# Kernel optimization log

Hardware: AMD Instinct MI355X
Metric: run time of the kernel (lower is better)

Reference implementation:

```python
import jax, jax.numpy as jnp
import numpy as np

M1 = 32
M2 = 32
S1 = 64
S2 = 64
TWO_PI = jnp.float32(2.0 * np.pi)


def setup_inputs() -> dict:
    key = jax.random.key(0)
    k1, k2, k3, k4, k5 = jax.random.split(key, 5)
    B, C, N = 8, 64, 16384
    x = jax.random.normal(k1, (B, C, N), dtype=jnp.float32)
    x_in = jax.random.uniform(k2, (B, N, 2), dtype=jnp.float32)
    x_out = jax.random.uniform(k3, (B, N, 2), dtype=jnp.float32)
    # xavier_normal for fan_in=64, fan_out=64 over [i,o,m,2]
    std = jnp.float32(np.sqrt(2.0 / (64 + 64)))
    w1 = std * jax.random.normal(k4, (64, 64, M2, 2), dtype=jnp.float32)
    w2 = std * jax.random.normal(k5, (64, 64, M1, 2), dtype=jnp.float32)
    return {"x": x, "x_in": x_in, "x_out": x_out, "w1": w1, "w2": w2}


def reference(x, x_in, x_out, w1, w2):
    # iphi = identity: mapped coords are the mesh coords themselves.
    # Original code repeats the 1-D NUFFT bases along the grid dims (s1/s2)
    # before the einsums; since the repeated axis is constant, the final
    # contraction over it is exactly a factor s1 (resp. s2). We compute the
    # mathematically identical form without materializing [B,N,m,s] tensors.
    Wy = w1[..., 0] + 1j * w1[..., 1]  # [i, o, m2] complex
    Wx = w2[..., 0] + 1j * w2[..., 1]  # [i, o, m1] complex
    ky = jnp.arange(M2, dtype=jnp.float32)
    kx = jnp.arange(M1, dtype=jnp.float32)

    # forward NUFFT bases from x_in  (exp(-i 2 pi k . p))
    bfy = jnp.exp(-1j * TWO_PI * x_in[..., 0:1] * ky)   # [B, N, m2]
    bfx = jnp.exp(-1j * TWO_PI * x_in[..., 1:2] * kx)   # [B, N, m1]
    # inverse NUFFT bases from x_out (exp(+i 2 pi k . p))
    ibfy = jnp.exp(1j * TWO_PI * x_out[..., 0:1] * ky)  # [B, N, m2]
    ibfx = jnp.exp(1j * TWO_PI * x_out[..., 1:2] * kx)  # [B, N, m1]

    xc = x.astype(jnp.complex64)

    # y-direction branch (fourier_weight[0])
    fty = jnp.einsum('bcn,bny->bcy', xc, bfy)           # [B, in, m2]
    my = jnp.einsum('biy,ioy->boy', fty, Wy)            # [B, out, m2]
    xy = S1 * jnp.einsum('boy,bny->bon', my, ibfy).real  # [B, out, N]

    # x-direction branch (fourier_weight[1])
    ftx = jnp.einsum('bcn,bnx->bcx', xc, bfx)           # [B, in, m1]
    mx = jnp.einsum('bix,iox->box', ftx, Wx)            # [B, out, m1]
    xx = S2 * jnp.einsum('box,bnx->bon', mx, ibfx).real  # [B, out, N]

    return xx + xy
```

## Files before the change

kernel.cpp:

```cpp
#include <hip/hip_runtime.h>

#define BB 8
#define CC 64
#define OO 64
#define NN 16384
#define MMODE 32
#define JJ 128
#define SFAC 64.0f

typedef __attribute__((ext_vector_type(8))) short short8;
typedef __attribute__((ext_vector_type(4))) float f32x4;

static __device__ __forceinline__ unsigned short f2bf(float f) {
  unsigned u = __float_as_uint(f);
  u += 0x7FFF + ((u >> 16) & 1);
  return (unsigned short)(u >> 16);
}
static __device__ __forceinline__ unsigned pack2(float a, float b) {
  return (unsigned)f2bf(a) | ((unsigned)f2bf(b) << 16);
}
static __device__ __forceinline__ float sin2pi(float x) { return __builtin_amdgcn_sinf(x); }
static __device__ __forceinline__ float cos2pi(float x) { return __builtin_amdgcn_cosf(x); }


__global__ __launch_bounds__(256) void fwd_kernel(
    const float* __restrict__ x, const float* __restrict__ x_in,
    float* __restrict__ part) {
  __shared__ __attribute__((aligned(16))) short bas[JJ * 72];
  __shared__ __attribute__((aligned(16))) short xs[32 * 72];
  __shared__ __attribute__((aligned(16))) float ps[1024];
  const int t = threadIdx.x;
  const int b = blockIdx.z, chalf = blockIdx.y, sl = blockIdx.x;
  const int n0 = sl * 512;

  {
    const float4 v = *(const float4*)&x_in[((size_t)b * NN + n0) * 2 + t * 4];
    *(float4*)&ps[t * 4] = v;
  }
  const int xc = t >> 3, xng = t & 7;
  const float* xbase = x + ((size_t)(b * CC + chalf * 32 + xc)) * NN + n0 + xng * 4;
  float4 ra = *(const float4*)(xbase);
  float4 rb = *(const float4*)(xbase + 32);

  const int w = t >> 6, L = t & 63;
  const int q4 = L >> 4, l15 = L & 15;
  f32x4 acc[4];
#pragma unroll
  for (int i = 0; i < 4; ++i) acc[i] = (f32x4){0.f, 0.f, 0.f, 0.f};

  __syncthreads();

  for (int s = 0; s < 8; ++s) {
    *(uint2*)&xs[xc * 72 + xng * 4]      = make_uint2(pack2(ra.x, ra.y), pack2(ra.z, ra.w));
    *(uint2*)&xs[xc * 72 + xng * 4 + 32] = make_uint2(pack2(rb.x, rb.y), pack2(rb.z, rb.w));
    if (s < 7) {
      ra = *(const float4*)(xbase + (s + 1) * 64);
      rb = *(const float4*)(xbase + (s + 1) * 64 + 32);
    }
#pragma unroll
    for (int ti = 0; ti < 2; ++ti) {
      const int tau = t + ti * 256;
      const int ng = tau & 7, mm = tau >> 3;
      const int br = mm >> 5, m = mm & 31;
      const float fm = (float)m;
      union { unsigned short u[8]; uint4 v; } R, I;
#pragma unroll
      for (int k = 0; k < 8; ++k) {
        const float p = ps[(s * 64 + ng * 8 + k) * 2 + br];
        float rev = fm * p;
        rev -= floorf(rev);
        R.u[k] = f2bf(cos2pi(rev));
        I.u[k] = f2bf(-sin2pi(rev));
      }
      const int row = br * 64 + 2 * m;
      *(uint4*)&bas[row * 72 + ng * 8]       = R.v;
      *(uint4*)&bas[(row + 1) * 72 + ng * 8] = I.v;
    }
    __syncthreads();
#pragma unroll
    for (int ks = 0; ks < 2; ++ks) {
      const int ko = ks * 32 + q4 * 8;
      const short8 a0 = *(const short8*)&bas[(w * 32 + l15) * 72 + ko];
      const short8 a1 = *(const short8*)&bas[(w * 32 + 16 + l15) * 72 + ko];
      const short8 b0 = *(const short8*)&xs[l15 * 72 + ko];
      const short8 b1 = *(const short8*)&xs[(16 + l15) * 72 + ko];
      acc[0] = __builtin_amdgcn_mfma_f32_16x16x32_bf16(a0, b0, acc[0], 0, 0, 0);
      acc[1] = __builtin_amdgcn_mfma_f32_16x16x32_bf16(a0, b1, acc[1], 0, 0, 0);
      acc[2] = __builtin_amdgcn_mfma_f32_16x16x32_bf16(a1, b0, acc[2], 0, 0, 0);
      acc[3] = __builtin_amdgcn_mfma_f32_16x16x32_bf16(a1, b1, acc[3], 0, 0, 0);
    }
    __syncthreads();
  }
  float* pp = part + (size_t)(b * 32 + sl) * JJ * CC;
  const int jb0 = w * 32 + q4 * 4;
  const int cb = chalf * 32 + l15;
#pragma unroll
  for (int ji = 0; ji < 2; ++ji)
#pragma unroll
    for (int ci = 0; ci < 2; ++ci) {
      const f32x4 v = acc[ji * 2 + ci];
#pragma unroll
      for (int r = 0; r < 4; ++r)
        pp[(jb0 + ji * 16 + r) * CC + cb + ci * 16] = v[r];
    }
}

__global__ __launch_bounds__(256) void mix_kernel(
    const float* __restrict__ part, const float* __restrict__ w1,
    const float* __restrict__ w2, float* __restrict__ A) {
  __shared__ float red[8][64];
  __shared__ float fre[64], fim[64];
  const int m = blockIdx.x, branch = blockIdx.y, b = blockIdx.z;
  const int t = threadIdx.x;
  const int c = t & 63, g = t >> 6;
  const int jb = branch * 64 + 2 * m;
  float pre = 0.f, pim = 0.f;
#pragma unroll
  for (int k = 0; k < 8; ++k) {
    const int sl = g + 4 * k;
    const float* pp = part + (size_t)(b * 32 + sl) * JJ * CC;
    pre += pp[jb * CC + c];
    pim += pp[(jb + 1) * CC + c];
  }
  red[g * 2][c] = pre;
  red[g * 2 + 1][c] = pim;
  __syncthreads();
  if (t < 64) {
    fre[t] = red[0][t] + red[2][t] + red[4][t] + red[6][t];
    fim[t] = red[1][t] + red[3][t] + red[5][t] + red[7][t];
  }
  __syncthreads();
  const float* w = branch ? w2 : w1;
  const int o = c;
  float ar = 0.f, ai = 0.f;
#pragma unroll 4
  for (int ii = 0; ii < 16; ++ii) {
    const int i = g * 16 + ii;
    const float2 wv = *(const float2*)&w[(((size_t)i * 64 + o) * MMODE + m) * 2];
    ar += fre[i] * wv.x - fim[i] * wv.y;
    ai += fre[i] * wv.y + fim[i] * wv.x;
  }
  red[g * 2][o] = ar;
  red[g * 2 + 1][o] = ai;
  __syncthreads();
  if (t < 64) {
    const float sr = red[0][t] + red[2][t] + red[4][t] + red[6][t];
    const float si = red[1][t] + red[3][t] + red[5][t] + red[7][t];
    *(float2*)&A[((size_t)b * OO + t) * JJ + jb] = make_float2(SFAC * sr, -SFAC * si);
  }
}

__global__ __launch_bounds__(256) void inv_kernel(
    const float* __restrict__ x_out, const float* __restrict__ A,
    float* __restrict__ out) {
  __shared__ __attribute__((aligned(16))) short As_s[OO * 136];
  __shared__ __attribute__((aligned(16))) short basn[64 * 136];
  __shared__ __attribute__((aligned(16))) float psI[512];
  const int t = threadIdx.x;
  const int b = blockIdx.y;
  const int n0 = blockIdx.x * 256;

  if (t < 128) {
    const float4 v = *(const float4*)&x_out[((size_t)b * NN + n0) * 2 + t * 4];
    *(float4*)&psI[t * 4] = v;
  }
#pragma unroll
  for (int idx = t; idx < 2048; idx += 256) {
    const int o = idx >> 5, j4 = idx & 31;
    const float4 v = *(const float4*)&A[((size_t)b * OO + o) * JJ + j4 * 4];
    *(uint2*)&As_s[o * 136 + j4 * 4] = make_uint2(pack2(v.x, v.y), pack2(v.z, v.w));
  }
  const int w = t >> 6, L = t & 63;
  const int q4 = L >> 4, l15 = L & 15;
  const int nl = t & 63, q = t >> 6, br = q >> 1, half = q & 1;
  const int ot0 = (w & 1) * 32;
  const int nt0 = (w >> 1) * 32;
  __syncthreads();

  for (int s = 0; s < 4; ++s) {
    {
      const float p = psI[(s * 64 + nl) * 2 + br];
      const float fr = p - floorf(p);
      const float s1 = sin2pi(fr), c1 = cos2pi(fr);
      float brr = 1.f, bii = 0.f;
      if (half) {
        float r = c1, qq = s1;
#pragma unroll
        for (int k = 0; k < 4; ++k) { const float nr = r*r - qq*qq, ni = 2.f*r*qq; r = nr; qq = ni; }
        brr = r; bii = qq;
      }
      short* bp = &basn[nl * 136 + br * 64 + half * 32];
#pragma unroll
      for (int g = 0; g < 4; ++g) {
        union { unsigned short u[8]; uint4 v; } P;
#pragma unroll
        for (int mi = 0; mi < 4; ++mi) {
          P.u[2 * mi]     = f2bf(brr);
          P.u[2 * mi + 1] = f2bf(bii);
          const float nr = brr * c1 - bii * s1, ni = brr * s1 + bii * c1;
          brr = nr; bii = ni;
        }
        *(uint4*)&bp[g * 8] = P.v;
      }
    }
    __syncthreads();
    f32x4 acc[4];
#pragma unroll
    for (int i = 0; i < 4; ++i) acc[i] = (f32x4){0.f, 0.f, 0.f, 0.f};
#pragma unroll
    for (int ks = 0; ks < 4; ++ks) {
      const int ko = ks * 32 + q4 * 8;
      const short8 a0 = *(const short8*)&As_s[(ot0 + l15) * 136 + ko];
      const short8 a1 = *(const short8*)&As_s[(ot0 + 16 + l15) * 136 + ko];
      const short8 b0 = *(const short8*)&basn[(nt0 + l15) * 136 + ko];
      const short8 b1 = *(const short8*)&basn[(nt0 + 16 + l15) * 136 + ko];
      acc[0] = __builtin_amdgcn_mfma_f32_16x16x32_bf16(a0, b0, acc[0], 0, 0, 0);
      acc[1] = __builtin_amdgcn_mfma_f32_16x16x32_bf16(a0, b1, acc[1], 0, 0, 0);
      acc[2] = __builtin_amdgcn_mfma_f32_16x16x32_bf16(a1, b0, acc[2], 0, 0, 0);
      acc[3] = __builtin_amdgcn_mfma_f32_16x16x32_bf16(a1, b1, acc[3], 0, 0, 0);
    }
    const int nbase = n0 + s * 64 + nt0 + l15;
#pragma unroll
    for (int oi = 0; oi < 2; ++oi)
#pragma unroll
      for (int ni = 0; ni < 2; ++ni) {
        const f32x4 v = acc[oi * 2 + ni];
#pragma unroll
        for (int r = 0; r < 4; ++r)
          out[((size_t)b * OO + ot0 + oi * 16 + q4 * 4 + r) * NN + nbase + ni * 16] = v[r];
      }
    __syncthreads();
  }
}

extern "C" void kernel_launch(void* const* d_in, const int* in_sizes, int n_in,
                              void* d_out, int out_size, void* d_ws, size_t ws_size,
                              hipStream_t stream) {
  const float* x     = (const float*)d_in[0];
  const float* x_in  = (const float*)d_in[1];
  const float* x_out = (const float*)d_in[2];
  const float* w1    = (const float*)d_in[3];
  const float* w2    = (const float*)d_in[4];
  float* out = (float*)d_out;
  float* part = (float*)d_ws;
  float* A = part + (size_t)BB * 32 * JJ * CC;

  fwd_kernel<<<dim3(32, 2, BB), 256, 0, stream>>>(x, x_in, part);
  mix_kernel<<<dim3(MMODE, 2, BB), 256, 0, stream>>>(part, w1, w2, A);
  inv_kernel<<<dim3(64, BB), 256, 0, stream>>>(x_out, A, out);
}
```

Measured before the change: 119.5 us.

## Cover all channels per forward block and reduce partials with atomics

The forward kernel now has each block handle all 64 channels over a 256-point slice, so the NUFFT basis is computed once per slice instead of once per channel half. Per-slice partial sums are no longer written to a workspace; they are accumulated directly into a zeroed per-batch Fourier-coefficient buffer with float atomicAdd. This shrinks the mix kernel's reduction to a plain load. In exchange it adds a memset launch, contention on 64-way atomics, and nondeterministic summation order.

```diff
diff --git a/kernel.cpp b/kernel.cpp
--- a/kernel.cpp
+++ b/kernel.cpp
@@ -25,37 +25,41 @@
 
 __global__ __launch_bounds__(256) void fwd_kernel(
     const float* __restrict__ x, const float* __restrict__ x_in,
-    float* __restrict__ part) {
+    float* __restrict__ ft) {
   __shared__ __attribute__((aligned(16))) short bas[JJ * 72];
-  __shared__ __attribute__((aligned(16))) short xs[32 * 72];
-  __shared__ __attribute__((aligned(16))) float ps[1024];
+  __shared__ __attribute__((aligned(16))) short xs[64 * 72];
+  __shared__ __attribute__((aligned(16))) float ps[512];
   const int t = threadIdx.x;
-  const int b = blockIdx.z, chalf = blockIdx.y, sl = blockIdx.x;
-  const int n0 = sl * 512;
-
-  {
+  const int b = blockIdx.y, sl = blockIdx.x;
+  const int n0 = sl * 256;
+
+  if (t < 128) {
     const float4 v = *(const float4*)&x_in[((size_t)b * NN + n0) * 2 + t * 4];
     *(float4*)&ps[t * 4] = v;
   }
-  const int xc = t >> 3, xng = t & 7;
-  const float* xbase = x + ((size_t)(b * CC + chalf * 32 + xc)) * NN + n0 + xng * 4;
-  float4 ra = *(const float4*)(xbase);
-  float4 rb = *(const float4*)(xbase + 32);
+  const int xc = t >> 2, xq = t & 3;
+  const float* xbase = x + ((size_t)(b * CC + xc)) * NN + n0;
+  float4 cur[4];
+#pragma unroll
+  for (int k = 0; k < 4; ++k) cur[k] = *(const float4*)&xbase[(k * 4 + xq) * 4];
 
   const int w = t >> 6, L = t & 63;
   const int q4 = L >> 4, l15 = L & 15;
-  f32x4 acc[4];
-#pragma unroll
-  for (int i = 0; i < 4; ++i) acc[i] = (f32x4){0.f, 0.f, 0.f, 0.f};
-
-  __syncthreads();
-
-  for (int s = 0; s < 8; ++s) {
-    *(uint2*)&xs[xc * 72 + xng * 4]      = make_uint2(pack2(ra.x, ra.y), pack2(ra.z, ra.w));
-    *(uint2*)&xs[xc * 72 + xng * 4 + 32] = make_uint2(pack2(rb.x, rb.y), pack2(rb.z, rb.w));
-    if (s < 7) {
-      ra = *(const float4*)(xbase + (s + 1) * 64);
-      rb = *(const float4*)(xbase + (s + 1) * 64 + 32);
+  f32x4 acc[8];
+#pragma unroll
+  for (int i = 0; i < 8; ++i) acc[i] = (f32x4){0.f, 0.f, 0.f, 0.f};
+
+  __syncthreads();
+
+  for (int s = 0; s < 4; ++s) {
+#pragma unroll
+    for (int k = 0; k < 4; ++k)
+      *(uint2*)&xs[xc * 72 + (k * 4 + xq) * 4] =
+          make_uint2(pack2(cur[k].x, cur[k].y), pack2(cur[k].z, cur[k].w));
+    if (s < 3) {
+#pragma unroll
+      for (int k = 0; k < 4; ++k)
+        cur[k] = *(const float4*)&xbase[(s + 1) * 64 + (k * 4 + xq) * 4];
     }
 #pragma unroll
     for (int ti = 0; ti < 2; ++ti) {
@@ -82,31 +86,28 @@
       const int ko = ks * 32 + q4 * 8;
       const short8 a0 = *(const short8*)&bas[(w * 32 + l15) * 72 + ko];
       const short8 a1 = *(const short8*)&bas[(w * 32 + 16 + l15) * 72 + ko];
-      const short8 b0 = *(const short8*)&xs[l15 * 72 + ko];
-      const short8 b1 = *(const short8*)&xs[(16 + l15) * 72 + ko];
-      acc[0] = __builtin_amdgcn_mfma_f32_16x16x32_bf16(a0, b0, acc[0], 0, 0, 0);
-      acc[1] = __builtin_amdgcn_mfma_f32_16x16x32_bf16(a0, b1, acc[1], 0, 0, 0);
-      acc[2] = __builtin_amdgcn_mfma_f32_16x16x32_bf16(a1, b0, acc[2], 0, 0, 0);
-      acc[3] = __builtin_amdgcn_mfma_f32_16x16x32_bf16(a1, b1, acc[3], 0, 0, 0);
-    }
-    __syncthreads();
-  }
-  float* pp = part + (size_t)(b * 32 + sl) * JJ * CC;
-  const int jb0 = w * 32 + q4 * 4;
-  const int cb = chalf * 32 + l15;
-#pragma unroll
-  for (int ji = 0; ji < 2; ++ji)
-#pragma unroll
-    for (int ci = 0; ci < 2; ++ci) {
-      const f32x4 v = acc[ji * 2 + ci];
+#pragma unroll
+      for (int ct = 0; ct < 4; ++ct) {
+        const short8 bv = *(const short8*)&xs[(ct * 16 + l15) * 72 + ko];
+        acc[ct]     = __builtin_amdgcn_mfma_f32_16x16x32_bf16(a0, bv, acc[ct], 0, 0, 0);
+        acc[4 + ct] = __builtin_amdgcn_mfma_f32_16x16x32_bf16(a1, bv, acc[4 + ct], 0, 0, 0);
+      }
+    }
+    __syncthreads();
+  }
+#pragma unroll
+  for (int ai = 0; ai < 2; ++ai)
+#pragma unroll
+    for (int ct = 0; ct < 4; ++ct) {
+      const f32x4 v = acc[ai * 4 + ct];
 #pragma unroll
       for (int r = 0; r < 4; ++r)
-        pp[(jb0 + ji * 16 + r) * CC + cb + ci * 16] = v[r];
+        atomicAdd(&ft[((size_t)b * JJ + w * 32 + ai * 16 + q4 * 4 + r) * CC + ct * 16 + l15], v[r]);
     }
 }
 
 __global__ __launch_bounds__(256) void mix_kernel(
-    const float* __restrict__ part, const float* __restrict__ w1,
+    const float* __restrict__ ft, const float* __restrict__ w1,
     const float* __restrict__ w2, float* __restrict__ A) {
   __shared__ float red[8][64];
   __shared__ float fre[64], fim[64];
@@ -114,34 +115,20 @@
   const int t = threadIdx.x;
   const int c = t & 63, g = t >> 6;
   const int jb = branch * 64 + 2 * m;
-  float pre = 0.f, pim = 0.f;
-#pragma unroll
-  for (int k = 0; k < 8; ++k) {
-    const int sl = g + 4 * k;
-    const float* pp = part + (size_t)(b * 32 + sl) * JJ * CC;
-    pre += pp[jb * CC + c];
-    pim += pp[(jb + 1) * CC + c];
-  }
-  red[g * 2][c] = pre;
-  red[g * 2 + 1][c] = pim;
-  __syncthreads();
-  if (t < 64) {
-    fre[t] = red[0][t] + red[2][t] + red[4][t] + red[6][t];
-    fim[t] = red[1][t] + red[3][t] + red[5][t] + red[7][t];
-  }
+  if (t < 64) fre[t] = ft[((size_t)b * JJ + jb) * CC + t];
+  else if (t < 128) fim[t - 64] = ft[((size_t)b * JJ + jb + 1) * CC + (t - 64)];
   __syncthreads();
   const float* w = branch ? w2 : w1;
-  const int o = c;
   float ar = 0.f, ai = 0.f;
 #pragma unroll 4
   for (int ii = 0; ii < 16; ++ii) {
     const int i = g * 16 + ii;
-    const float2 wv = *(const float2*)&w[(((size_t)i * 64 + o) * MMODE + m) * 2];
+    const float2 wv = *(const float2*)&w[(((size_t)i * 64 + c) * MMODE + m) * 2];
     ar += fre[i] * wv.x - fim[i] * wv.y;
     ai += fre[i] * wv.y + fim[i] * wv.x;
   }
-  red[g * 2][o] = ar;
-  red[g * 2 + 1][o] = ai;
+  red[g * 2][c] = ar;
+  red[g * 2 + 1][c] = ai;
   __syncthreads();
   if (t < 64) {
     const float sr = red[0][t] + red[2][t] + red[4][t] + red[6][t];
@@ -242,10 +229,11 @@
   const float* w1    = (const float*)d_in[3];
   const float* w2    = (const float*)d_in[4];
   float* out = (float*)d_out;
-  float* part = (float*)d_ws;
-  float* A = part + (size_t)BB * 32 * JJ * CC;
-
-  fwd_kernel<<<dim3(32, 2, BB), 256, 0, stream>>>(x, x_in, part);
-  mix_kernel<<<dim3(MMODE, 2, BB), 256, 0, stream>>>(part, w1, w2, A);
+  float* ft = (float*)d_ws;
+  float* A  = ft + (size_t)BB * JJ * CC;
+
+  hipMemsetAsync(ft, 0, (size_t)BB * JJ * CC * sizeof(float), stream);
+  fwd_kernel<<<dim3(64, BB), 256, 0, stream>>>(x, x_in, ft);
+  mix_kernel<<<dim3(MMODE, 2, BB), 256, 0, stream>>>(ft, w1, w2, A);
   inv_kernel<<<dim3(64, BB), 256, 0, stream>>>(x_out, A, out);
 }
```

New measurement: 125.5 us. 5.1% more time.
